# Optimization experiments

Hardware: AMD Instinct MI355X
Metric: run time of the kernel (lower is better)

## Reference

```python
import jax, jax.numpy as jnp
import numpy as np

N_SAMPLES = 8388608  # total packed samples across all rays
N_RAYS = 131072      # number of rays (segments)


def setup_inputs() -> dict:
    key = jax.random.key(0)
    k1, k2, k3 = jax.random.split(key, 3)
    # Sorted segment ids emulate the packed ray layout (samples of a ray are contiguous).
    segment_ids = jnp.sort(
        jax.random.randint(k1, (N_SAMPLES,), 0, N_RAYS, dtype=jnp.int32)
    )
    rgb_samples = jax.random.normal(k2, (N_SAMPLES, 3), dtype=jnp.float32)
    weights_samples = jax.random.uniform(k3, (N_SAMPLES, 1), dtype=jnp.float32)
    return {
        "segment_ids": segment_ids,
        "rgb_samples": rgb_samples,
        "weights_samples": weights_samples,
        "n_rays": N_RAYS,
    }


def reference(segment_ids, rgb_samples, weights_samples, n_rays):
    # pred_rgb[r] = sum over samples s belonging to ray r of w_s * rgb_s
    weighted = rgb_samples * weights_samples  # [N,3], weight broadcast over channels
    pred_rgb = jax.ops.segment_sum(weighted, segment_ids, num_segments=n_rays)  # [n_rays,3]
    return pred_rgb
```

## Files before the change

### kernel.cpp

```cpp
#include <hip/hip_runtime.h>


#define NTHREADS 256
#define WAVES_PER_BLOCK (NTHREADS / 64)
#define CPL 4
#define CHUNK (64 * CPL)
#define CHUNKS 8
#define SPW (CHUNK * CHUNKS)
#define CHUNK_BYTES (CHUNK * 20)
#define IDS_OFF 0
#define W_OFF 1024
#define RGB_OFF 2048

__global__ __launch_bounds__(NTHREADS) void zero_out_kernel(float4* __restrict__ out4,
                                                            int n4) {
  int i = blockIdx.x * blockDim.x + threadIdx.x;
  if (i < n4) out4[i] = make_float4(0.f, 0.f, 0.f, 0.f);
}

__device__ __forceinline__ void gll16(const void* g, void* l) {
  __builtin_amdgcn_global_load_lds(
      (const __attribute__((address_space(1))) void*)g,
      (__attribute__((address_space(3))) void*)l, 16, 0, 0);
}

__device__ __forceinline__ void process_chunk(const int4 id4, const float4 w4,
                                              const float4 r0, const float4 r1,
                                              const float4 r2, const int lane,
                                              float* __restrict__ out) {
  int idv[CPL] = {id4.x, id4.y, id4.z, id4.w};
  float px[CPL], py[CPL], pz[CPL];
  px[0] = r0.x * w4.x; py[0] = r0.y * w4.x; pz[0] = r0.z * w4.x;
  px[1] = r0.w * w4.y; py[1] = r1.x * w4.y; pz[1] = r1.y * w4.y;
  px[2] = r1.z * w4.z; py[2] = r1.w * w4.z; pz[2] = r2.x * w4.z;
  px[3] = r2.y * w4.w; py[3] = r2.z * w4.w; pz[3] = r2.w * w4.w;

  const int first_id = idv[0];
  int run_id = first_id;
  float rx = px[0], ry = py[0], rz = pz[0];
  float hx = 0.f, hy = 0.f, hz = 0.f;
  bool f_intra = false;
  #pragma unroll
  for (int k = 1; k < CPL; ++k) {
    if (idv[k] == run_id) {
      rx += px[k]; ry += py[k]; rz += pz[k];
    } else {
      if (!f_intra) {
        hx = rx; hy = ry; hz = rz; f_intra = true;
      } else {
        atomicAdd(&out[3 * run_id + 0], rx);
        atomicAdd(&out[3 * run_id + 1], ry);
        atomicAdd(&out[3 * run_id + 2], rz);
      }
      run_id = idv[k];
      rx = px[k]; ry = py[k]; rz = pz[k];
    }
  }
  const int last_id = run_id;

  const int prev_tid = __shfl_up(last_id, 1, 64);
  int fl = (lane == 0 || f_intra || prev_tid != first_id) ? 1 : 0;
  float sx = rx, sy = ry, sz = rz;
  #pragma unroll
  for (int off = 1; off < 64; off <<= 1) {
    const float ox = __shfl_up(sx, off, 64);
    const float oy = __shfl_up(sy, off, 64);
    const float oz = __shfl_up(sz, off, 64);
    const int ofl = __shfl_up(fl, off, 64);
    if (lane >= off && fl == 0) { sx += ox; sy += oy; sz += oz; fl = ofl; }
  }

  const float pSx = __shfl_up(sx, 1, 64);
  const float pSy = __shfl_up(sy, 1, 64);
  const float pSz = __shfl_up(sz, 1, 64);
  if (f_intra) {
    const bool link = (lane > 0) && (prev_tid == first_id);
    atomicAdd(&out[3 * first_id + 0], hx + (link ? pSx : 0.f));
    atomicAdd(&out[3 * first_id + 1], hy + (link ? pSy : 0.f));
    atomicAdd(&out[3 * first_id + 2], hz + (link ? pSz : 0.f));
  }

  const int next_hid = __shfl_down(first_id, 1, 64);
  if (lane == 63 || next_hid != last_id) {
    atomicAdd(&out[3 * last_id + 0], sx);
    atomicAdd(&out[3 * last_id + 1], sy);
    atomicAdd(&out[3 * last_id + 2], sz);
  }
}

__global__ __launch_bounds__(NTHREADS) void integrate_kernel(
    const int* __restrict__ ids, const float* __restrict__ rgb,
    const float* __restrict__ w, float* __restrict__ out, int n_samples) {
  __shared__ char lds[WAVES_PER_BLOCK * 2 * CHUNK_BYTES];
  const int lane = threadIdx.x & 63;
  const int wib = threadIdx.x >> 6;
  char* mybuf = lds + wib * (2 * CHUNK_BYTES);

  const long long wave_id = (long long)blockIdx.x * WAVES_PER_BLOCK + wib;
  const long long span0 = wave_id * SPW;
  if (span0 >= (long long)n_samples) return;

  if (span0 + SPW <= (long long)n_samples) {
    const char* gid = (const char*)(ids + span0) + lane * 16;
    const char* gw  = (const char*)(w + span0) + lane * 16;
    const char* grg = (const char*)(rgb + 3 * span0) + lane * 16;

#define STAGE(c, b)                                                     \
    do {                                                                \
      const long long o_ = (long long)(c) * (CHUNK * 4);                \
      char* lb_ = mybuf + (b) * CHUNK_BYTES;                            \
      gll16(gid + o_, lb_ + IDS_OFF);                                   \
      gll16(gw + o_, lb_ + W_OFF);                                      \
      gll16(grg + 3 * o_, lb_ + RGB_OFF);                               \
      gll16(grg + 3 * o_ + 1024, lb_ + RGB_OFF + 1024);                 \
      gll16(grg + 3 * o_ + 2048, lb_ + RGB_OFF + 2048);                 \
    } while (0)

    STAGE(0, 0);
    STAGE(1, 1);
    #pragma unroll
    for (int c = 0; c < CHUNKS; ++c) {
      if (c < CHUNKS - 1) {
        asm volatile("s_waitcnt vmcnt(5)" ::: "memory");
      } else {
        asm volatile("s_waitcnt vmcnt(0)" ::: "memory");
      }
      const char* lb = mybuf + (c & 1) * CHUNK_BYTES;
      const int4   i4 = *(const int4*)(lb + IDS_OFF + lane * 16);
      const float4 w4 = *(const float4*)(lb + W_OFF + lane * 16);
      const float4 r0 = *(const float4*)(lb + RGB_OFF + lane * 48);
      const float4 r1 = *(const float4*)(lb + RGB_OFF + lane * 48 + 16);
      const float4 r2 = *(const float4*)(lb + RGB_OFF + lane * 48 + 32);
      process_chunk(i4, w4, r0, r1, r2, lane, out);
      if (c + 2 < CHUNKS) {
        asm volatile("s_waitcnt lgkmcnt(0)" ::: "memory");
        STAGE(c + 2, c & 1);
      }
    }
#undef STAGE
  } else {
    const int last = ids[n_samples - 1];
    for (int c = 0; c < CHUNKS; ++c) {
      const long long cb = span0 + (long long)c * CHUNK;
      if (cb >= (long long)n_samples) break;
      int idt[CPL]; float wt[CPL], rt[3 * CPL];
      #pragma unroll
      for (int j = 0; j < CPL; ++j) {
        const long long s = cb + (long long)lane * CPL + j;
        if (s < (long long)n_samples) {
          idt[j] = ids[s];
          wt[j] = w[s];
          rt[3 * j + 0] = rgb[3 * s + 0];
          rt[3 * j + 1] = rgb[3 * s + 1];
          rt[3 * j + 2] = rgb[3 * s + 2];
        } else {
          idt[j] = (j == 0) ? last : idt[j - 1];
          wt[j] = 0.f;
          rt[3 * j + 0] = rt[3 * j + 1] = rt[3 * j + 2] = 0.f;
        }
      }
      const int4 i4 = make_int4(idt[0], idt[1], idt[2], idt[3]);
      const float4 w4 = make_float4(wt[0], wt[1], wt[2], wt[3]);
      const float4 r0 = make_float4(rt[0], rt[1], rt[2], rt[3]);
      const float4 r1 = make_float4(rt[4], rt[5], rt[6], rt[7]);
      const float4 r2 = make_float4(rt[8], rt[9], rt[10], rt[11]);
      process_chunk(i4, w4, r0, r1, r2, lane, out);
    }
  }
}

extern "C" void kernel_launch(void* const* d_in, const int* in_sizes, int n_in,
                              void* d_out, int out_size, void* d_ws, size_t ws_size,
                              hipStream_t stream) {
  const int*   segment_ids = (const int*)d_in[0];
  const float* rgb         = (const float*)d_in[1];
  const float* weights     = (const float*)d_in[2];
  float*       out         = (float*)d_out;

  const int n_samples = in_sizes[0];

  {
    int n4 = out_size / 4;
    int blocks = (n4 + NTHREADS - 1) / NTHREADS;
    zero_out_kernel<<<blocks, NTHREADS, 0, stream>>>((float4*)out, n4);
  }
  {
    long long waves = ((long long)n_samples + SPW - 1) / SPW;
    int blocks = (int)((waves + WAVES_PER_BLOCK - 1) / WAVES_PER_BLOCK);
    integrate_kernel<<<blocks, NTHREADS, 0, stream>>>(
        segment_ids, rgb, weights, out, n_samples);
  }
}
```

Measured before the change: 202.2 us.

## Carry wave-tail partial sums across chunks and buffer atomics in registers

The main path now carries lane 63's run sum into the next chunk, so a ray spanning a chunk boundary is merged in registers instead of taking extra atomics. The first two atomic pushes per lane are held in register slots and flushed only at kernel end, which spreads the atomic traffic out. The zero-init kernel is replaced by hipMemsetAsync, the chunk loop is no longer unrolled, and launch bounds now request 4 blocks per CU. The extra live registers and branching may hurt occupancy or add divergence.

```diff
diff --git a/kernel.cpp b/kernel.cpp
--- a/kernel.cpp
+++ b/kernel.cpp
@@ -12,22 +12,15 @@
 #define W_OFF 1024
 #define RGB_OFF 2048
 
-__global__ __launch_bounds__(NTHREADS) void zero_out_kernel(float4* __restrict__ out4,
-                                                            int n4) {
-  int i = blockIdx.x * blockDim.x + threadIdx.x;
-  if (i < n4) out4[i] = make_float4(0.f, 0.f, 0.f, 0.f);
-}
-
 __device__ __forceinline__ void gll16(const void* g, void* l) {
   __builtin_amdgcn_global_load_lds(
       (const __attribute__((address_space(1))) void*)g,
       (__attribute__((address_space(3))) void*)l, 16, 0, 0);
 }
 
-__device__ __forceinline__ void process_chunk(const int4 id4, const float4 w4,
-                                              const float4 r0, const float4 r1,
-                                              const float4 r2, const int lane,
-                                              float* __restrict__ out) {
+__device__ __forceinline__ void process_chunk_tailpath(
+    const int4 id4, const float4 w4, const float4 r0, const float4 r1,
+    const float4 r2, const int lane, float* __restrict__ out) {
   int idv[CPL] = {id4.x, id4.y, id4.z, id4.w};
   float px[CPL], py[CPL], pz[CPL];
   px[0] = r0.x * w4.x; py[0] = r0.y * w4.x; pz[0] = r0.z * w4.x;
@@ -45,9 +38,8 @@
     if (idv[k] == run_id) {
       rx += px[k]; ry += py[k]; rz += pz[k];
     } else {
-      if (!f_intra) {
-        hx = rx; hy = ry; hz = rz; f_intra = true;
-      } else {
+      if (!f_intra) { hx = rx; hy = ry; hz = rz; f_intra = true; }
+      else {
         atomicAdd(&out[3 * run_id + 0], rx);
         atomicAdd(&out[3 * run_id + 1], ry);
         atomicAdd(&out[3 * run_id + 2], rz);
@@ -79,7 +71,6 @@
     atomicAdd(&out[3 * first_id + 1], hy + (link ? pSy : 0.f));
     atomicAdd(&out[3 * first_id + 2], hz + (link ? pSz : 0.f));
   }
-
   const int next_hid = __shfl_down(first_id, 1, 64);
   if (lane == 63 || next_hid != last_id) {
     atomicAdd(&out[3 * last_id + 0], sx);
@@ -88,7 +79,7 @@
   }
 }
 
-__global__ __launch_bounds__(NTHREADS) void integrate_kernel(
+__global__ __launch_bounds__(NTHREADS, 4) void integrate_kernel(
     const int* __restrict__ ids, const float* __restrict__ rgb,
     const float* __restrict__ w, float* __restrict__ out, int n_samples) {
   __shared__ char lds[WAVES_PER_BLOCK * 2 * CHUNK_BYTES];
@@ -99,6 +90,19 @@
   const long long wave_id = (long long)blockIdx.x * WAVES_PER_BLOCK + wib;
   const long long span0 = wave_id * SPW;
   if (span0 >= (long long)n_samples) return;
+
+  int s0id = -1, s1id = -1;
+  float s0x = 0.f, s0y = 0.f, s0z = 0.f, s1x = 0.f, s1y = 0.f, s1z = 0.f;
+#define PUSH(pid, pxv, pyv, pzv)                                        \
+  do {                                                                  \
+    if (s0id < 0)      { s0id = (pid); s0x = (pxv); s0y = (pyv); s0z = (pzv); } \
+    else if (s1id < 0) { s1id = (pid); s1x = (pxv); s1y = (pyv); s1z = (pzv); } \
+    else {                              \
+      atomicAdd(&out[3 * (pid) + 0], (pxv));                            \
+      atomicAdd(&out[3 * (pid) + 1], (pyv));                            \
+      atomicAdd(&out[3 * (pid) + 2], (pzv));                            \
+    }                                                                   \
+  } while (0)
 
   if (span0 + SPW <= (long long)n_samples) {
     const char* gid = (const char*)(ids + span0) + lane * 16;
@@ -118,7 +122,10 @@
 
     STAGE(0, 0);
     STAGE(1, 1);
-    #pragma unroll
+
+    int cid = -1;
+    float cx = 0.f, cy = 0.f, cz = 0.f;
+
     for (int c = 0; c < CHUNKS; ++c) {
       if (c < CHUNKS - 1) {
         asm volatile("s_waitcnt vmcnt(5)" ::: "memory");
@@ -131,13 +138,77 @@
       const float4 r0 = *(const float4*)(lb + RGB_OFF + lane * 48);
       const float4 r1 = *(const float4*)(lb + RGB_OFF + lane * 48 + 16);
       const float4 r2 = *(const float4*)(lb + RGB_OFF + lane * 48 + 32);
-      process_chunk(i4, w4, r0, r1, r2, lane, out);
+
+      int idv[CPL] = {i4.x, i4.y, i4.z, i4.w};
+      float px[CPL], py[CPL], pz[CPL];
+      px[0] = r0.x * w4.x; py[0] = r0.y * w4.x; pz[0] = r0.z * w4.x;
+      px[1] = r0.w * w4.y; py[1] = r1.x * w4.y; pz[1] = r1.y * w4.y;
+      px[2] = r1.z * w4.z; py[2] = r1.w * w4.z; pz[2] = r2.x * w4.z;
+      px[3] = r2.y * w4.w; py[3] = r2.z * w4.w; pz[3] = r2.w * w4.w;
+
+      const int first_id = idv[0];
+      int run_id = first_id;
+      float rx = px[0], ry = py[0], rz = pz[0];
+      float hx = 0.f, hy = 0.f, hz = 0.f;
+      bool f_intra = false;
+      #pragma unroll
+      for (int k = 1; k < CPL; ++k) {
+        if (idv[k] == run_id) {
+          rx += px[k]; ry += py[k]; rz += pz[k];
+        } else {
+          if (!f_intra) { hx = rx; hy = ry; hz = rz; f_intra = true; }
+          else          { PUSH(run_id, rx, ry, rz); }
+          run_id = idv[k];
+          rx = px[k]; ry = py[k]; rz = pz[k];
+        }
+      }
+      const int last_id = run_id;
+
+      if (lane == 0 && cid >= 0) {
+        if (cid == first_id) {
+          if (f_intra) { hx += cx; hy += cy; hz += cz; }
+          else         { rx += cx; ry += cy; rz += cz; }
+        } else {
+          PUSH(cid, cx, cy, cz);
+        }
+      }
+
+      const int prev_tid = __shfl_up(last_id, 1, 64);
+      int fl = (lane == 0 || f_intra || prev_tid != first_id) ? 1 : 0;
+      float sx = rx, sy = ry, sz = rz;
+      #pragma unroll
+      for (int off = 1; off < 64; off <<= 1) {
+        const float ox = __shfl_up(sx, off, 64);
+        const float oy = __shfl_up(sy, off, 64);
+        const float oz = __shfl_up(sz, off, 64);
+        const int ofl = __shfl_up(fl, off, 64);
+        if (lane >= off && fl == 0) { sx += ox; sy += oy; sz += oz; fl = ofl; }
+      }
+
+      const float pSx = __shfl_up(sx, 1, 64);
+      const float pSy = __shfl_up(sy, 1, 64);
+      const float pSz = __shfl_up(sz, 1, 64);
+      if (f_intra) {
+        const bool link = (lane > 0) && (prev_tid == first_id);
+        PUSH(first_id, hx + (link ? pSx : 0.f), hy + (link ? pSy : 0.f),
+             hz + (link ? pSz : 0.f));
+      }
+
+      const int next_hid = __shfl_down(first_id, 1, 64);
+      if (lane < 63 && next_hid != last_id) PUSH(last_id, sx, sy, sz);
+      cid = __shfl(last_id, 63, 64);
+      cx = __shfl(sx, 63, 64);
+      cy = __shfl(sy, 63, 64);
+      cz = __shfl(sz, 63, 64);
+
       if (c + 2 < CHUNKS) {
         asm volatile("s_waitcnt lgkmcnt(0)" ::: "memory");
         STAGE(c + 2, c & 1);
       }
     }
 #undef STAGE
+
+    if (lane == 0 && cid >= 0) PUSH(cid, cx, cy, cz);
   } else {
     const int last = ids[n_samples - 1];
     for (int c = 0; c < CHUNKS; ++c) {
@@ -164,9 +235,21 @@
       const float4 r0 = make_float4(rt[0], rt[1], rt[2], rt[3]);
       const float4 r1 = make_float4(rt[4], rt[5], rt[6], rt[7]);
       const float4 r2 = make_float4(rt[8], rt[9], rt[10], rt[11]);
-      process_chunk(i4, w4, r0, r1, r2, lane, out);
+      process_chunk_tailpath(i4, w4, r0, r1, r2, lane, out);
     }
   }
+
+  if (s0id >= 0) {
+    atomicAdd(&out[3 * s0id + 0], s0x);
+    atomicAdd(&out[3 * s0id + 1], s0y);
+    atomicAdd(&out[3 * s0id + 2], s0z);
+  }
+  if (s1id >= 0) {
+    atomicAdd(&out[3 * s1id + 0], s1x);
+    atomicAdd(&out[3 * s1id + 1], s1y);
+    atomicAdd(&out[3 * s1id + 2], s1z);
+  }
+#undef PUSH
 }
 
 extern "C" void kernel_launch(void* const* d_in, const int* in_sizes, int n_in,
@@ -179,15 +262,10 @@
 
   const int n_samples = in_sizes[0];
 
-  {
-    int n4 = out_size / 4;
-    int blocks = (n4 + NTHREADS - 1) / NTHREADS;
-    zero_out_kernel<<<blocks, NTHREADS, 0, stream>>>((float4*)out, n4);
-  }
-  {
-    long long waves = ((long long)n_samples + SPW - 1) / SPW;
-    int blocks = (int)((waves + WAVES_PER_BLOCK - 1) / WAVES_PER_BLOCK);
-    integrate_kernel<<<blocks, NTHREADS, 0, stream>>>(
-        segment_ids, rgb, weights, out, n_samples);
-  }
-}
+  hipMemsetAsync(out, 0, out_size, stream);
+
+  long long waves = ((long long)n_samples + SPW - 1) / SPW;
+  int blocks = (int)((waves + WAVES_PER_BLOCK - 1) / WAVES_PER_BLOCK);
+  integrate_kernel<<<blocks, NTHREADS, 0, stream>>>(
+      segment_ids, rgb, weights, out, n_samples);
+}
```

Measured after the change: 204.6 us. Within noise of the previous version (+1.2%).
